# Optimization experiments

Measured on AMD Instinct MI355X. Metric: run time of the kernel, lower is better.

Reference implementation:

```python
import jax, jax.numpy as jnp
import numpy as np


def _log_g(x):
    # log of g(x) where g(x) = relu(x)+0.5 for x>=0 else sigmoid(x)
    return jnp.where(x >= 0, jnp.log(jax.nn.relu(x) + 0.5), -jax.nn.softplus(-x))


def _mingru(inp, h_prev, W, b):
    """Log-space parallel minGRU scan.
    inp: (B,S,Din), h_prev: (B,1,H), W: (2H,Din), b: (2H,) -> (B,S,H)
    """
    gh = jnp.einsum('bsd,ed->bse', inp, W) + b  # (B,S,2H)
    gate, hidden = jnp.split(gh, 2, axis=-1)
    log_coeffs = -jax.nn.softplus(gate)    # log(1 - z_t)
    log_z = -jax.nn.softplus(-gate)        # log z_t
    B, S, H = hidden.shape
    a_star = jnp.concatenate(
        [jnp.zeros((B, 1, H), gate.dtype), jnp.cumsum(log_coeffs, axis=1)], axis=1)  # (B,S+1,H)
    log_values = jnp.concatenate([_log_g(h_prev), log_z + _log_g(hidden)], axis=1)   # (B,S+1,H)
    log_h = a_star + jax.lax.cumlogsumexp(log_values - a_star, axis=1)
    return jnp.exp(log_h)[:, 1:]  # (B,S,H)


def setup_inputs() -> dict:
    key = jax.random.key(0)
    k0, k1, k2 = jax.random.split(key, 3)
    B, S, D, H, L = 8, 2048, 1024, 1024, 4
    x = jax.random.normal(k0, (B, S, D), jnp.float32)
    h = jnp.zeros((L, B, 1, H), jnp.float32)
    W0 = jax.random.normal(k1, (2 * H, D), jnp.float32) * 0.02
    b0 = jnp.zeros((2 * H,), jnp.float32)
    Wl = jax.random.normal(k2, (L - 1, 2 * H, H), jnp.float32) * 0.02
    bl = jnp.zeros((L - 1, 2 * H), jnp.float32)
    return {"x": x, "h": h, "W0": W0, "b0": b0, "Wl": Wl, "bl": bl}


def reference(x, h, W0, b0, Wl, bl):
    num_layers = h.shape[0]
    inp = x
    finals = []
    out = inp
    for lidx in range(num_layers):
        W = W0 if lidx == 0 else Wl[lidx - 1]
        b = b0 if lidx == 0 else bl[lidx - 1]
        out = _mingru(inp, h[lidx], W, b)
        finals.append(out[:, -1:])
        # residual: align is Identity since input_dims == hidden_dims
        out = out + inp
        # dropout == 0.0 -> no mask applied (matches original branch)
        inp = out
    return out, jnp.stack(finals)
```

## Files before the change

### kernel.cpp

```cpp
#include <hip/hip_runtime.h>
#include <hip/hip_bf16.h>

using bf16 = __hip_bfloat16;
typedef __bf16 bf16x8 __attribute__((ext_vector_type(8)));
typedef __bf16 bf16x4 __attribute__((ext_vector_type(4)));
typedef __bf16 bf16x2 __attribute__((ext_vector_type(2)));
typedef float  f32x4  __attribute__((ext_vector_type(4)));

#define B_ 8
#define S_ 2048
#define H_ 1024
#define M_ (B_ * S_)
#define N_ (2 * H_)
#define K_ 1024
#define CHUNKS_ 32
#define CLEN_ 64

__device__ __forceinline__ bf16x8 load8f(const float* p) {
  const float4 a = *(const float4*)p;
  const float4 b = *(const float4*)(p + 4);
  bf16x8 r;
  r[0] = (__bf16)a.x; r[1] = (__bf16)a.y; r[2] = (__bf16)a.z; r[3] = (__bf16)a.w;
  r[4] = (__bf16)b.x; r[5] = (__bf16)b.y; r[6] = (__bf16)b.z; r[7] = (__bf16)b.w;
  return r;
}

__global__ __launch_bounds__(256)
void cvt_f32_bf16(const float* __restrict__ src, bf16* __restrict__ dst, long n) {
  const long i = ((long)blockIdx.x * 256 + threadIdx.x) * 8;
  if (i >= n) return;
  *(bf16x8*)(dst + i) = load8f(src + i);
}

template <bool WDMA>
__global__ __launch_bounds__(256)
void gemm_bias(const bf16* __restrict__ A, const bf16* __restrict__ Wb,
               const float* __restrict__ Wf, const float* __restrict__ bias,
               bf16* __restrict__ C) {
  __shared__ __align__(16) char lds[16384];
  const int tid  = threadIdx.x;
  const int lane = tid & 63;
  const int wv   = tid >> 6;
  const int wr   = wv >> 1;
  const int wc   = wv & 1;
  const int r15  = lane & 15;
  const int kq   = lane >> 4;
  const int mBase = blockIdx.y * 128;
  const int nBase = blockIdx.x * 128;

  f32x4 acc[4][4];
#pragma unroll
  for (int i = 0; i < 4; ++i)
#pragma unroll
    for (int j = 0; j < 4; ++j)
#pragma unroll
      for (int r = 0; r < 4; ++r) acc[i][j][r] = 0.0f;

  for (int k0 = 0; k0 < K_; k0 += 32) {
    bf16x8 sw[2];
    if constexpr (!WDMA) {
#pragma unroll
      for (int c = 0; c < 2; ++c) {
        const int seg = wv * 2 + c;
        sw[c] = load8f(Wf + (size_t)(nBase + seg * 16 + r15) * K_ + k0 + kq * 8);
      }
    }
    __syncthreads();
#pragma unroll
    for (int c = 0; c < 2; ++c) {
      const int seg = wv * 2 + c;
      const bf16* ga = A + (size_t)(mBase + seg * 16 + r15) * K_ + k0 + kq * 8;
      __builtin_amdgcn_global_load_lds(
          (const __attribute__((address_space(1))) void*)ga,
          (__attribute__((address_space(3))) void*)(lds + seg * 1024), 16, 0, 0);
      if constexpr (WDMA) {
        const bf16* gw = Wb + (size_t)(nBase + seg * 16 + r15) * K_ + k0 + kq * 8;
        __builtin_amdgcn_global_load_lds(
            (const __attribute__((address_space(1))) void*)gw,
            (__attribute__((address_space(3))) void*)(lds + 8192 + seg * 1024), 16, 0, 0);
      } else {
        *(bf16x8*)(lds + 8192 + seg * 1024 + lane * 16) = sw[c];
      }
    }
    __syncthreads();

    bf16x8 af[4], bfr[4];
#pragma unroll
    for (int i = 0; i < 4; ++i)
      af[i] = *(const bf16x8*)(lds + (wr * 4 + i) * 1024 + lane * 16);
#pragma unroll
    for (int j = 0; j < 4; ++j)
      bfr[j] = *(const bf16x8*)(lds + 8192 + (wc * 4 + j) * 1024 + lane * 16);
#pragma unroll
    for (int i = 0; i < 4; ++i)
#pragma unroll
      for (int j = 0; j < 4; ++j)
        acc[i][j] = __builtin_amdgcn_mfma_f32_16x16x32_bf16(af[i], bfr[j],
                                                            acc[i][j], 0, 0, 0);
  }

#pragma unroll
  for (int j = 0; j < 4; ++j) {
    const int col = nBase + wc * 64 + j * 16 + r15;
    const float bv = bias[col];
#pragma unroll
    for (int i = 0; i < 4; ++i) {
      const int row = mBase + wr * 64 + i * 16 + kq * 4;
#pragma unroll
      for (int r = 0; r < 4; ++r)
        C[(size_t)(row + r) * N_ + col] = __float2bfloat16(acc[i][j][r] + bv);
    }
  }
}

#define BK_    64
#define NT_    (K_ / BK_)
#define LBUF_  65536
#define LBOFF_ 32768
#define LHALF_ 16384

__global__ __launch_bounds__(512, 2)
void gemm256(const bf16* __restrict__ A, const bf16* __restrict__ W,
             const float* __restrict__ bias, bf16* __restrict__ C) {
  __shared__ __align__(16) char lds[131072];
  const int tid  = threadIdx.x;
  const int lane = tid & 63;
  const int wv   = tid >> 6;
  const int wm   = wv >> 2;
  const int wn   = wv & 3;
  const int r15  = lane & 15;
  const int kq   = lane >> 4;

  const int flat = blockIdx.x;
  const int sw   = (flat & 7) * 64 + (flat >> 3);
  const int by   = sw >> 3;
  const int bx   = sw & 7;
  const int mBase = by * 256;
  const int nBase = bx * 256;

  size_t srcOff[2];
  int dstOff[2];
#pragma unroll
  for (int q = 0; q < 2; ++q) {
    const int t  = q * 512 + tid;
    const int cc = (t & 7) ^ ((t >> 3) & 7);
    srcOff[q] = (size_t)(t >> 3) * K_ + cc * 8;
    dstOff[q] = q * 8192 + wv * 1024;
  }
  const bf16* aH[2] = {A + (size_t)mBase * K_, A + (size_t)(mBase + 128) * K_};
  const bf16* wH[2] = {W + (size_t)nBase * K_, W + (size_t)(nBase + 128) * K_};

#define STAGE(GB, LOFF)                                                        \
  { _Pragma("unroll") for (int q_ = 0; q_ < 2; ++q_)                           \
      __builtin_amdgcn_global_load_lds(                                        \
          (const __attribute__((address_space(1))) void*)((GB) + srcOff[q_]),  \
          (__attribute__((address_space(3))) void*)(lds + (LOFF) + dstOff[q_]),\
          16, 0, 0); }

  const int xsw  = (r15 & 7) << 4;
  const int col0 = (kq * 16) ^ xsw;
  const int col1 = (64 + kq * 16) ^ xsw;
  const int aRow = wm * LHALF_ + r15 * 128;
  const int bRow = LBOFF_ + (wn >> 1) * LHALF_ + ((wn & 1) * 64 + r15) * 128;

  f32x4 acc[8][4];
#pragma unroll
  for (int i = 0; i < 8; ++i)
#pragma unroll
    for (int j = 0; j < 4; ++j)
#pragma unroll
      for (int r = 0; r < 4; ++r) acc[i][j][r] = 0.0f;

  bf16x8 aF[4][2], bF[4][2];

#define LD_A(BO)                                                               \
  { _Pragma("unroll") for (int i_ = 0; i_ < 4; ++i_) {                         \
      aF[i_][0] = *(const bf16x8*)(lds + (BO) + i_ * 2048 + col0);             \
      aF[i_][1] = *(const bf16x8*)(lds + (BO) + i_ * 2048 + col1); } }

#define LD_B(J0, BO)                                                           \
  { _Pragma("unroll") for (int j_ = 0; j_ < 2; ++j_) {                         \
      bF[(J0) + j_][0] =                                                       \
          *(const bf16x8*)(lds + (BO) + bRow + ((J0) + j_) * 2048 + col0);     \
      bF[(J0) + j_][1] =                                                       \
          *(const bf16x8*)(lds + (BO) + bRow + ((J0) + j_) * 2048 + col1); } }

#define MFMA_Q(I0, J0)                                                         \
  { _Pragma("unroll") for (int i_ = 0; i_ < 4; ++i_)                           \
    _Pragma("unroll") for (int j_ = 0; j_ < 2; ++j_)                           \
    _Pragma("unroll") for (int k_ = 0; k_ < 2; ++k_)                           \
      acc[(I0) + i_][(J0) + j_] = __builtin_amdgcn_mfma_f32_16x16x32_bf16(     \
          aF[i_][k_], bF[(J0) + j_][k_], acc[(I0) + i_][(J0) + j_], 0, 0, 0); }

#define PH_BAR()                                                               \
  __builtin_amdgcn_sched_barrier(0);                                           \
  __builtin_amdgcn_s_barrier();                                                \
  asm volatile("s_waitcnt lgkmcnt(0)" ::: "memory");                           \
  __builtin_amdgcn_sched_barrier(0);                                           \
  __builtin_amdgcn_s_setprio(1);

#define PH_END()                                                               \
  __builtin_amdgcn_s_setprio(0);                                               \
  __builtin_amdgcn_sched_barrier(0);                                           \
  __builtin_amdgcn_s_barrier();

#define PH_END_VM(N)                                                           \
  __builtin_amdgcn_s_setprio(0);                                               \
  __builtin_amdgcn_sched_barrier(0);                                           \
  asm volatile("s_waitcnt vmcnt(" #N ")" ::: "memory");                        \
  __builtin_amdgcn_s_barrier();

  STAGE(aH[0], 0);
  STAGE(aH[1], LHALF_);
  STAGE(wH[0], LBOFF_);
  STAGE(wH[1], LBOFF_ + LHALF_);
  STAGE(wH[0] + BK_, LBUF_ + LBOFF_);
  STAGE(aH[0] + BK_, LBUF_);
  asm volatile("s_waitcnt vmcnt(4)" ::: "memory");
  __builtin_amdgcn_s_barrier();

#pragma unroll 1
  for (int t = 0; t < NT_ - 2; t += 2) {
    const int o1 = (t + 1) * BK_, o2 = (t + 2) * BK_, o3 = (t + 3) * BK_;
    LD_A(aRow); LD_B(0, 0);
    STAGE(aH[1] + o1, LBUF_ + LHALF_);
    asm volatile("s_waitcnt lgkmcnt(8)" ::: "memory");
    PH_BAR(); MFMA_Q(0, 0); PH_END();
    LD_B(2, 0);
    STAGE(wH[1] + o1, LBUF_ + LBOFF_ + LHALF_);
    PH_BAR(); MFMA_Q(0, 2); PH_END();
    LD_A(aRow + 8192);
    STAGE(wH[0] + o2, LBOFF_);
    PH_BAR(); MFMA_Q(4, 0); PH_END();
    STAGE(aH[0] + o2, 0);
    PH_BAR(); MFMA_Q(4, 2); PH_END_VM(4);
    LD_A(LBUF_ + aRow); LD_B(0, LBUF_);
    STAGE(aH[1] + o2, LHALF_);
    asm volatile("s_waitcnt lgkmcnt(8)" ::: "memory");
    PH_BAR(); MFMA_Q(0, 0); PH_END();
    LD_B(2, LBUF_);
    STAGE(wH[1] + o2, LBOFF_ + LHALF_);
    PH_BAR(); MFMA_Q(0, 2); PH_END();
    LD_A(LBUF_ + aRow + 8192);
    STAGE(wH[0] + o3, LBUF_ + LBOFF_);
    PH_BAR(); MFMA_Q(4, 0); PH_END();
    STAGE(aH[0] + o3, LBUF_);
    PH_BAR(); MFMA_Q(4, 2); PH_END_VM(4);
  }

  {
    const int o1 = (NT_ - 1) * BK_;
    LD_A(aRow); LD_B(0, 0);
    STAGE(aH[1] + o1, LBUF_ + LHALF_);
    asm volatile("s_waitcnt lgkmcnt(8)" ::: "memory");
    PH_BAR(); MFMA_Q(0, 0); PH_END();
    LD_B(2, 0);
    STAGE(wH[1] + o1, LBUF_ + LBOFF_ + LHALF_);
    PH_BAR(); MFMA_Q(0, 2); PH_END();
    LD_A(aRow + 8192);
    PH_BAR(); MFMA_Q(4, 0); PH_END();
    PH_BAR(); MFMA_Q(4, 2); PH_END_VM(0);
    LD_A(LBUF_ + aRow); LD_B(0, LBUF_);
    PH_BAR(); MFMA_Q(0, 0); PH_END();
    LD_B(2, LBUF_);
    PH_BAR(); MFMA_Q(0, 2); PH_END();
    LD_A(LBUF_ + aRow + 8192);
    PH_BAR(); MFMA_Q(4, 0); PH_END();
    PH_BAR(); MFMA_Q(4, 2);
    __builtin_amdgcn_s_setprio(0);
  }

#pragma unroll
  for (int j = 0; j < 4; ++j) {
    const int col = nBase + wn * 64 + j * 16 + r15;
    const float bv = bias[col];
#pragma unroll
    for (int i = 0; i < 8; ++i) {
      const int row0 = mBase + wm * 128 + i * 16 + kq * 4;
#pragma unroll
      for (int r = 0; r < 4; ++r)
        C[(size_t)(row0 + r) * N_ + col] = __float2bfloat16(acc[i][j][r] + bv);
    }
  }
#undef STAGE
#undef LD_A
#undef LD_B
#undef MFMA_Q
#undef PH_BAR
#undef PH_END
#undef PH_END_VM
}

__device__ __forceinline__ float rcpf(float x) { return __builtin_amdgcn_rcpf(x); }

__device__ __forceinline__ void step_coeffs(float gate, float hidden,
                                            float& ca, float& cb) {
  const float e1 = __expf(gate);
  ca = rcpf(1.0f + e1);
  const float z = 1.0f - ca;
  float g;
  if (hidden >= 0.0f) {
    g = hidden + 0.5f;
  } else {
    const float e2 = __expf(hidden);
    g = e2 * rcpf(1.0f + e2);
  }
  cb = z * g;
}

__device__ __forceinline__ float g_of(float x) {
  if (x >= 0.0f) return x + 0.5f;
  const float e = __expf(x);
  return e * rcpf(1.0f + e);
}

__global__ __launch_bounds__(256)
void scan_chunk(const bf16* __restrict__ gh, float2* __restrict__ sAB) {
  const int tx = threadIdx.x, bx = blockIdx.x;
  const int half = bx & 1, b = (bx >> 1) & 7, j = bx >> 4;
  const int h = half * 512 + tx * 2;
  const int c = b * 1024 + h;
  const bf16* gbase = gh + ((size_t)(b * S_ + j * CLEN_)) * N_ + h;
  float A0 = 1.0f, B0 = 0.0f, A1 = 1.0f, B1 = 0.0f;
#pragma unroll 8
  for (int t = 0; t < CLEN_; ++t) {
    const bf16x2 gv = *(const bf16x2*)(gbase + (size_t)t * N_);
    const bf16x2 hv = *(const bf16x2*)(gbase + (size_t)t * N_ + H_);
    float ca, cb;
    step_coeffs((float)gv[0], (float)hv[0], ca, cb);
    A0 *= ca;  B0 = ca * B0 + cb;
    step_coeffs((float)gv[1], (float)hv[1], ca, cb);
    A1 *= ca;  B1 = ca * B1 + cb;
  }
  *(float4*)(sAB + (size_t)j * (B_ * H_) + c) = make_float4(A0, B0, A1, B1);
}

__global__ __launch_bounds__(256)
void scan_apply(const bf16* __restrict__ gh, const float2* __restrict__ sAB,
                const float* __restrict__ hprev,
                const float* rin, float* rout, bf16* __restrict__ gout,
                float* __restrict__ finals) {
  const int tx = threadIdx.x, bx = blockIdx.x;
  const int half = bx & 1, b = (bx >> 1) & 7, j = bx >> 4;
  const int h = half * 512 + tx * 2;
  const int c = b * 1024 + h;

  float h0, h1;
  {
    const float2 hp = *(const float2*)(hprev + c);
    h0 = g_of(hp.x); h1 = g_of(hp.y);
  }
  for (int jj = 0; jj < j; ++jj) {
    const float4 ab = *(const float4*)(sAB + (size_t)jj * (B_ * H_) + c);
    h0 = ab.x * h0 + ab.y;
    h1 = ab.z * h1 + ab.w;
  }

  const size_t rbase = ((size_t)(b * S_ + j * CLEN_)) * H_ + h;
  const bf16* gbase = gh + ((size_t)(b * S_ + j * CLEN_)) * N_ + h;
#pragma unroll 1
  for (int tt = 0; tt < CLEN_; tt += 8) {
    bf16x2 gv[8], hv[8];
    float2 rv[8];
#pragma unroll
    for (int u = 0; u < 8; ++u) {
      const size_t t = (size_t)(tt + u);
      gv[u] = *(const bf16x2*)(gbase + t * N_);
      hv[u] = *(const bf16x2*)(gbase + t * N_ + H_);
      rv[u] = *(const float2*)(rin + rbase + t * H_);
    }
#pragma unroll
    for (int u = 0; u < 8; ++u) {
      const size_t t = (size_t)(tt + u);
      float ca, cb;
      step_coeffs((float)gv[u][0], (float)hv[u][0], ca, cb);
      h0 = ca * h0 + cb;
      step_coeffs((float)gv[u][1], (float)hv[u][1], ca, cb);
      h1 = ca * h1 + cb;
      const float r0 = h0 + rv[u].x;
      const float r1 = h1 + rv[u].y;
      *(float2*)(rout + rbase + t * H_) = make_float2(r0, r1);
      if (gout) {
        bf16x2 o;
        o[0] = (__bf16)r0; o[1] = (__bf16)r1;
        *(bf16x2*)(gout + rbase + t * H_) = o;
      }
    }
  }
  if (j == CHUNKS_ - 1)
    *(float2*)(finals + c) = make_float2(h0, h1);
}

extern "C" void kernel_launch(void* const* d_in, const int* in_sizes, int n_in,
                              void* d_out, int out_size, void* d_ws,
                              size_t ws_size, hipStream_t stream) {
  const float* x  = (const float*)d_in[0];
  const float* h0 = (const float*)d_in[1];
  const float* W0 = (const float*)d_in[2];
  const float* b0 = (const float*)d_in[3];
  const float* Wl = (const float*)d_in[4];
  const float* bl = (const float*)d_in[5];
  float* out    = (float*)d_out;
  float* finals = out + (size_t)M_ * H_;

  char* ws = (char*)d_ws;
  bf16* gh   = (bf16*)ws;
  bf16* bufA = (bf16*)(ws + (64u << 20));

  const bool wide = ws_size >= ((size_t)115 << 20);
  bf16*   wb    = wide ? (bf16*)(ws + (96u << 20)) : nullptr;
  float2* sAB   = (float2*)(ws + ((wide ? 112u : 96u) << 20));

  cvt_f32_bf16<<<dim3(M_ * K_ / 8 / 256), 256, 0, stream>>>(x, bufA, (long)M_ * K_);
  if (wide) {
    cvt_f32_bf16<<<dim3(N_ * K_ / 8 / 256), 256, 0, stream>>>(W0, wb, (long)N_ * K_);
    cvt_f32_bf16<<<dim3(3 * N_ * K_ / 8 / 256), 256, 0, stream>>>(
        Wl, wb + (size_t)N_ * K_, (long)3 * N_ * K_);
  }

  for (int l = 0; l < 4; ++l) {
    const float* Wf = (l == 0) ? W0 : Wl + (size_t)(l - 1) * N_ * K_;
    const float* bi = (l == 0) ? b0 : bl + (size_t)(l - 1) * N_;
    if (wide) {
      gemm256<<<dim3(512), 512, 0, stream>>>(
          bufA, wb + (size_t)l * N_ * K_, bi, gh);
    } else {
      gemm_bias<false><<<dim3(16, 128), 256, 0, stream>>>(
          bufA, nullptr, Wf, bi, gh);
    }
    scan_chunk<<<dim3(512), 256, 0, stream>>>(gh, sAB);
    scan_apply<<<dim3(512), 256, 0, stream>>>(
        gh, sAB, h0 + (size_t)l * B_ * H_, (l == 0) ? x : out, out,
        (l == 3) ? nullptr : bufA, finals + (size_t)l * B_ * H_);
  }
}
```

Before: 672.9 us.

## Fuse gate coefficient computation and chunk scan into GEMM epilogue with interleaved weights

Weight rows are permuted at conversion so each wave's 64 output columns hold matching gate and hidden columns. The GEMM epilogue then computes the per-step coefficients (a,b) directly, stores them as bf16, and reduces per-chunk (A,B) scan summaries through cross-lane shuffles, which removes the separate scan_chunk kernel. scan_apply now reads the precomputed coefficients and no longer evaluates exp or reciprocal. The trade is a heavier GEMM epilogue with more register pressure, and the coefficients are rounded to bf16 before the recurrence; the fallback gemm_bias path is dropped in favour of per-layer weight packing.

```diff
diff --git a/kernel.cpp b/kernel.cpp
--- a/kernel.cpp
+++ b/kernel.cpp
@@ -32,85 +32,42 @@
   *(bf16x8*)(dst + i) = load8f(src + i);
 }
 
-template <bool WDMA>
 __global__ __launch_bounds__(256)
-void gemm_bias(const bf16* __restrict__ A, const bf16* __restrict__ Wb,
-               const float* __restrict__ Wf, const float* __restrict__ bias,
-               bf16* __restrict__ C) {
-  __shared__ __align__(16) char lds[16384];
-  const int tid  = threadIdx.x;
-  const int lane = tid & 63;
-  const int wv   = tid >> 6;
-  const int wr   = wv >> 1;
-  const int wc   = wv & 1;
-  const int r15  = lane & 15;
-  const int kq   = lane >> 4;
-  const int mBase = blockIdx.y * 128;
-  const int nBase = blockIdx.x * 128;
-
-  f32x4 acc[4][4];
-#pragma unroll
-  for (int i = 0; i < 4; ++i)
-#pragma unroll
-    for (int j = 0; j < 4; ++j)
-#pragma unroll
-      for (int r = 0; r < 4; ++r) acc[i][j][r] = 0.0f;
-
-  for (int k0 = 0; k0 < K_; k0 += 32) {
-    bf16x8 sw[2];
-    if constexpr (!WDMA) {
-#pragma unroll
-      for (int c = 0; c < 2; ++c) {
-        const int seg = wv * 2 + c;
-        sw[c] = load8f(Wf + (size_t)(nBase + seg * 16 + r15) * K_ + k0 + kq * 8);
-      }
-    }
-    __syncthreads();
-#pragma unroll
-    for (int c = 0; c < 2; ++c) {
-      const int seg = wv * 2 + c;
-      const bf16* ga = A + (size_t)(mBase + seg * 16 + r15) * K_ + k0 + kq * 8;
-      __builtin_amdgcn_global_load_lds(
-          (const __attribute__((address_space(1))) void*)ga,
-          (__attribute__((address_space(3))) void*)(lds + seg * 1024), 16, 0, 0);
-      if constexpr (WDMA) {
-        const bf16* gw = Wb + (size_t)(nBase + seg * 16 + r15) * K_ + k0 + kq * 8;
-        __builtin_amdgcn_global_load_lds(
-            (const __attribute__((address_space(1))) void*)gw,
-            (__attribute__((address_space(3))) void*)(lds + 8192 + seg * 1024), 16, 0, 0);
-      } else {
-        *(bf16x8*)(lds + 8192 + seg * 1024 + lane * 16) = sw[c];
-      }
-    }
-    __syncthreads();
-
-    bf16x8 af[4], bfr[4];
-#pragma unroll
-    for (int i = 0; i < 4; ++i)
-      af[i] = *(const bf16x8*)(lds + (wr * 4 + i) * 1024 + lane * 16);
-#pragma unroll
-    for (int j = 0; j < 4; ++j)
-      bfr[j] = *(const bf16x8*)(lds + 8192 + (wc * 4 + j) * 1024 + lane * 16);
-#pragma unroll
-    for (int i = 0; i < 4; ++i)
-#pragma unroll
-      for (int j = 0; j < 4; ++j)
-        acc[i][j] = __builtin_amdgcn_mfma_f32_16x16x32_bf16(af[i], bfr[j],
-                                                            acc[i][j], 0, 0, 0);
-  }
-
-#pragma unroll
-  for (int j = 0; j < 4; ++j) {
-    const int col = nBase + wc * 64 + j * 16 + r15;
-    const float bv = bias[col];
-#pragma unroll
-    for (int i = 0; i < 4; ++i) {
-      const int row = mBase + wr * 64 + i * 16 + kq * 4;
-#pragma unroll
-      for (int r = 0; r < 4; ++r)
-        C[(size_t)(row + r) * N_ + col] = __float2bfloat16(acc[i][j][r] + bv);
-    }
-  }
+void cvt_pack_w(const float* __restrict__ src, bf16* __restrict__ dst, int nmat) {
+  const long idx = (long)blockIdx.x * 256 + threadIdx.x;
+  const long e = idx * 8;
+  if (e >= (long)nmat * N_ * K_) return;
+  const int m = (int)(e / ((long)N_ * K_));
+  const long em = e - (long)m * N_ * K_;
+  const int prow = (int)(em >> 10);
+  const int col  = (int)(em & (K_ - 1));
+  const int g = prow >> 5, ty = (prow >> 4) & 1, u = prow & 15;
+  const int orow = ty * H_ + g * 16 + u;
+  *(bf16x8*)(dst + ((long)m * N_ + prow) * K_ + col) =
+      load8f(src + ((long)m * N_ + orow) * K_ + col);
+}
+
+__device__ __forceinline__ float rcpf(float x) { return __builtin_amdgcn_rcpf(x); }
+
+__device__ __forceinline__ void step_coeffs(float gate, float hidden,
+                                            float& ca, float& cb) {
+  const float e1 = __expf(gate);
+  ca = rcpf(1.0f + e1);
+  const float z = 1.0f - ca;
+  float g;
+  if (hidden >= 0.0f) {
+    g = hidden + 0.5f;
+  } else {
+    const float e2 = __expf(hidden);
+    g = e2 * rcpf(1.0f + e2);
+  }
+  cb = z * g;
+}
+
+__device__ __forceinline__ float g_of(float x) {
+  if (x >= 0.0f) return x + 0.5f;
+  const float e = __expf(x);
+  return e * rcpf(1.0f + e);
 }
 
 #define BK_    64
@@ -121,7 +78,8 @@
 
 __global__ __launch_bounds__(512, 2)
 void gemm256(const bf16* __restrict__ A, const bf16* __restrict__ W,
-             const float* __restrict__ bias, bf16* __restrict__ C) {
+             const float* __restrict__ bias, bf16* __restrict__ C,
+             float2* __restrict__ sAB) {
   __shared__ __align__(16) char lds[131072];
   const int tid  = threadIdx.x;
   const int lane = tid & 63;
@@ -270,16 +228,75 @@
     __builtin_amdgcn_s_setprio(0);
   }
 
-#pragma unroll
-  for (int j = 0; j < 4; ++j) {
-    const int col = nBase + wn * 64 + j * 16 + r15;
-    const float bv = bias[col];
+  const int colBase = nBase + wn * 64;
+  const int x0 = (colBase >> 1) + r15;
+  const int x1 = x0 + 16;
+  const float bg0 = bias[x0], bh0 = bias[H_ + x0];
+  const float bg1 = bias[x1], bh1 = bias[H_ + x1];
+
+  float segA[2][8], segB[2][8];
+#pragma unroll
+  for (int i = 0; i < 8; ++i) {
+    float A0 = 1.f, B0 = 0.f, A1 = 1.f, B1 = 0.f;
+    const size_t rw0 = (size_t)(mBase + wm * 128 + i * 16 + kq * 4) * N_;
+#pragma unroll
+    for (int r = 0; r < 4; ++r) {
+      float ca0, cb0, ca1, cb1;
+      step_coeffs(acc[i][0][r] + bg0, acc[i][1][r] + bh0, ca0, cb0);
+      step_coeffs(acc[i][2][r] + bg1, acc[i][3][r] + bh1, ca1, cb1);
+      const bf16 qa0 = __float2bfloat16(ca0), qb0 = __float2bfloat16(cb0);
+      const bf16 qa1 = __float2bfloat16(ca1), qb1 = __float2bfloat16(cb1);
+      const size_t rw = rw0 + (size_t)r * N_;
+      C[rw + colBase + r15]      = qa0;
+      C[rw + colBase + 16 + r15] = qb0;
+      C[rw + colBase + 32 + r15] = qa1;
+      C[rw + colBase + 48 + r15] = qb1;
+      const float fa0 = __bfloat162float(qa0), fb0 = __bfloat162float(qb0);
+      const float fa1 = __bfloat162float(qa1), fb1 = __bfloat162float(qb1);
+      A0 = fa0 * A0; B0 = fa0 * B0 + fb0;
+      A1 = fa1 * A1; B1 = fa1 * B1 + fb1;
+    }
+    segA[0][i] = A0; segB[0][i] = B0;
+    segA[1][i] = A1; segB[1][i] = B1;
+  }
+
+#pragma unroll
+  for (int ch = 0; ch < 2; ++ch)
 #pragma unroll
     for (int i = 0; i < 8; ++i) {
-      const int row0 = mBase + wm * 128 + i * 16 + kq * 4;
-#pragma unroll
-      for (int r = 0; r < 4; ++r)
-        C[(size_t)(row0 + r) * N_ + col] = __float2bfloat16(acc[i][j][r] + bv);
+      float A = segA[ch][i], Bv = segB[ch][i];
+      {
+        const float pA = __shfl_xor(A, 16, 64);
+        const float pB = __shfl_xor(Bv, 16, 64);
+        Bv = (lane & 16) ? (A * pB + Bv) : (pA * Bv + pB);
+        A = A * pA;
+      }
+      {
+        const float pA = __shfl_xor(A, 32, 64);
+        const float pB = __shfl_xor(Bv, 32, 64);
+        Bv = (lane & 32) ? (A * pB + Bv) : (pA * Bv + pB);
+        A = A * pA;
+      }
+      segA[ch][i] = A; segB[ch][i] = Bv;
+    }
+
+  if (kq == 0) {
+    const int b_idx = mBase / S_;
+    const int j0 = ((mBase % S_) + wm * 128) / 64;
+#pragma unroll
+    for (int c = 0; c < 2; ++c) {
+#pragma unroll
+      for (int ch = 0; ch < 2; ++ch) {
+        float A = 1.f, Bv = 0.f;
+#pragma unroll
+        for (int i = 4 * c; i < 4 * c + 4; ++i) {
+          A = segA[ch][i] * A;
+          Bv = segA[ch][i] * Bv + segB[ch][i];
+        }
+        const int x = (ch == 0) ? x0 : x1;
+        sAB[(size_t)(j0 + c) * (B_ * H_) + b_idx * 1024 + x] =
+            make_float2(A, Bv);
+      }
     }
   }
 #undef STAGE
@@ -289,50 +306,6 @@
 #undef PH_BAR
 #undef PH_END
 #undef PH_END_VM
-}
-
-__device__ __forceinline__ float rcpf(float x) { return __builtin_amdgcn_rcpf(x); }
-
-__device__ __forceinline__ void step_coeffs(float gate, float hidden,
-                                            float& ca, float& cb) {
-  const float e1 = __expf(gate);
-  ca = rcpf(1.0f + e1);
-  const float z = 1.0f - ca;
-  float g;
-  if (hidden >= 0.0f) {
-    g = hidden + 0.5f;
-  } else {
-    const float e2 = __expf(hidden);
-    g = e2 * rcpf(1.0f + e2);
-  }
-  cb = z * g;
-}
-
-__device__ __forceinline__ float g_of(float x) {
-  if (x >= 0.0f) return x + 0.5f;
-  const float e = __expf(x);
-  return e * rcpf(1.0f + e);
-}
-
-__global__ __launch_bounds__(256)
-void scan_chunk(const bf16* __restrict__ gh, float2* __restrict__ sAB) {
-  const int tx = threadIdx.x, bx = blockIdx.x;
-  const int half = bx & 1, b = (bx >> 1) & 7, j = bx >> 4;
-  const int h = half * 512 + tx * 2;
-  const int c = b * 1024 + h;
-  const bf16* gbase = gh + ((size_t)(b * S_ + j * CLEN_)) * N_ + h;
-  float A0 = 1.0f, B0 = 0.0f, A1 = 1.0f, B1 = 0.0f;
-#pragma unroll 8
-  for (int t = 0; t < CLEN_; ++t) {
-    const bf16x2 gv = *(const bf16x2*)(gbase + (size_t)t * N_);
-    const bf16x2 hv = *(const bf16x2*)(gbase + (size_t)t * N_ + H_);
-    float ca, cb;
-    step_coeffs((float)gv[0], (float)hv[0], ca, cb);
-    A0 *= ca;  B0 = ca * B0 + cb;
-    step_coeffs((float)gv[1], (float)hv[1], ca, cb);
-    A1 *= ca;  B1 = ca * B1 + cb;
-  }
-  *(float4*)(sAB + (size_t)j * (B_ * H_) + c) = make_float4(A0, B0, A1, B1);
 }
 
 __global__ __launch_bounds__(256)
@@ -344,6 +317,7 @@
   const int half = bx & 1, b = (bx >> 1) & 7, j = bx >> 4;
   const int h = half * 512 + tx * 2;
   const int c = b * 1024 + h;
+  const int pc = h + ((h >> 4) << 4);
 
   float h0, h1;
   {
@@ -357,26 +331,23 @@
   }
 
   const size_t rbase = ((size_t)(b * S_ + j * CLEN_)) * H_ + h;
-  const bf16* gbase = gh + ((size_t)(b * S_ + j * CLEN_)) * N_ + h;
+  const bf16* gbase = gh + ((size_t)(b * S_ + j * CLEN_)) * N_ + pc;
 #pragma unroll 1
   for (int tt = 0; tt < CLEN_; tt += 8) {
-    bf16x2 gv[8], hv[8];
+    bf16x2 av[8], bv[8];
     float2 rv[8];
 #pragma unroll
     for (int u = 0; u < 8; ++u) {
       const size_t t = (size_t)(tt + u);
-      gv[u] = *(const bf16x2*)(gbase + t * N_);
-      hv[u] = *(const bf16x2*)(gbase + t * N_ + H_);
+      av[u] = *(const bf16x2*)(gbase + t * N_);
+      bv[u] = *(const bf16x2*)(gbase + t * N_ + 16);
       rv[u] = *(const float2*)(rin + rbase + t * H_);
     }
 #pragma unroll
     for (int u = 0; u < 8; ++u) {
       const size_t t = (size_t)(tt + u);
-      float ca, cb;
-      step_coeffs((float)gv[u][0], (float)hv[u][0], ca, cb);
-      h0 = ca * h0 + cb;
-      step_coeffs((float)gv[u][1], (float)hv[u][1], ca, cb);
-      h1 = ca * h1 + cb;
+      h0 = (float)av[u][0] * h0 + (float)bv[u][0];
+      h1 = (float)av[u][1] * h1 + (float)bv[u][1];
       const float r0 = h0 + rv[u].x;
       const float r1 = h1 + rv[u].y;
       *(float2*)(rout + rbase + t * H_) = make_float2(r0, r1);
@@ -408,27 +379,27 @@
   bf16* bufA = (bf16*)(ws + (64u << 20));
 
   const bool wide = ws_size >= ((size_t)115 << 20);
-  bf16*   wb    = wide ? (bf16*)(ws + (96u << 20)) : nullptr;
-  float2* sAB   = (float2*)(ws + ((wide ? 112u : 96u) << 20));
+  bf16*   wb  = (bf16*)(ws + (96u << 20));
+  float2* sAB = (float2*)(ws + ((wide ? 112u : 101u) << 20));
 
   cvt_f32_bf16<<<dim3(M_ * K_ / 8 / 256), 256, 0, stream>>>(x, bufA, (long)M_ * K_);
   if (wide) {
-    cvt_f32_bf16<<<dim3(N_ * K_ / 8 / 256), 256, 0, stream>>>(W0, wb, (long)N_ * K_);
-    cvt_f32_bf16<<<dim3(3 * N_ * K_ / 8 / 256), 256, 0, stream>>>(
-        Wl, wb + (size_t)N_ * K_, (long)3 * N_ * K_);
+    cvt_pack_w<<<dim3(N_ * K_ / 8 / 256), 256, 0, stream>>>(W0, wb, 1);
+    cvt_pack_w<<<dim3(3 * N_ * K_ / 8 / 256), 256, 0, stream>>>(
+        Wl, wb + (size_t)N_ * K_, 3);
   }
 
   for (int l = 0; l < 4; ++l) {
     const float* Wf = (l == 0) ? W0 : Wl + (size_t)(l - 1) * N_ * K_;
     const float* bi = (l == 0) ? b0 : bl + (size_t)(l - 1) * N_;
+    bf16* wl_ptr;
     if (wide) {
-      gemm256<<<dim3(512), 512, 0, stream>>>(
-          bufA, wb + (size_t)l * N_ * K_, bi, gh);
+      wl_ptr = wb + (size_t)l * N_ * K_;
     } else {
-      gemm_bias<false><<<dim3(16, 128), 256, 0, stream>>>(
-          bufA, nullptr, Wf, bi, gh);
-    }
-    scan_chunk<<<dim3(512), 256, 0, stream>>>(gh, sAB);
+      cvt_pack_w<<<dim3(N_ * K_ / 8 / 256), 256, 0, stream>>>(Wf, wb, 1);
+      wl_ptr = wb;
+    }
+    gemm256<<<dim3(512), 512, 0, stream>>>(bufA, wl_ptr, bi, gh, sAB);
     scan_apply<<<dim3(512), 256, 0, stream>>>(
         gh, sAB, h0 + (size_t)l * B_ * H_, (l == 0) ? x : out, out,
         (l == 3) ? nullptr : bufA, finals + (size_t)l * B_ * H_);
```

Result: faster. 565.9 us (-15.9%).
